# Kernel optimization log

Measured on AMD Instinct MI355X. Metric: run time of the kernel, lower is better.

Reference implementation:

```python
import jax, jax.numpy as jnp
import numpy as np

FEATURE_DIM = 1024
N_CONCEPTS = 32768
BATCH = 1024
TEMPERATURE = 0.1
EPS = 1e-12  # matches torch F.normalize eps


def l2_normalize(x, axis=-1):
    n = jnp.linalg.norm(x, axis=axis, keepdims=True)
    return x / jnp.maximum(n, EPS)


def setup_inputs() -> dict:
    key = jax.random.key(0)
    k1, k2, k3, k4 = jax.random.split(key, 4)
    features = jax.random.normal(k1, (BATCH, FEATURE_DIM), dtype=jnp.float32)
    # Linear projection params (original inits to identity/zeros; random exercises the math)
    W = jnp.eye(FEATURE_DIM, dtype=jnp.float32) + 0.02 * jax.random.normal(k2, (FEATURE_DIM, FEATURE_DIM), dtype=jnp.float32)
    b = 0.01 * jax.random.normal(k3, (FEATURE_DIM,), dtype=jnp.float32)
    prototypes = l2_normalize(jax.random.normal(k4, (N_CONCEPTS, FEATURE_DIM), dtype=jnp.float32))
    return {"features": features, "W": W, "b": b, "prototypes": prototypes}


def reference(features, W, b, prototypes):
    # projection: features @ W.T + b   (torch nn.Linear convention)
    projected = jnp.einsum('bd,ed->be', features, W) + b          # [B, D]
    projected = l2_normalize(projected)                           # [B, D]
    # cosine similarity against all prototypes
    similarities = jnp.einsum('bd,kd->bk', projected, prototypes) # [B, K]
    activations = jax.nn.softmax(similarities / TEMPERATURE, axis=-1)
    best_idx = jnp.argmax(similarities, axis=-1)                  # [B] int
    return activations, best_idx
```

## Files before the change

kernel.cpp:

```cpp
#include <hip/hip_runtime.h>
#include <hip/hip_bf16.h>


typedef __attribute__((ext_vector_type(8))) short short8;
typedef __attribute__((ext_vector_type(4))) float floatx4;

__device__ __forceinline__ unsigned short f2bf(float f) {
  unsigned int u = __float_as_uint(f);
  u += 0x7fffu + ((u >> 16) & 1u);
  return (unsigned short)(u >> 16);
}
__device__ __forceinline__ float bf2f(unsigned short h) {
  return __uint_as_float(((unsigned int)h) << 16);
}

__global__ __launch_bounds__(256) void cvt_f32_bf16(
    const float* __restrict__ src, unsigned short* __restrict__ dst, int n8) {
  int i = blockIdx.x * blockDim.x + threadIdx.x;
  if (i >= n8) return;
  const float4* s4 = (const float4*)src;
  float4 a = s4[2 * i];
  float4 b = s4[2 * i + 1];
  short8 o;
  o[0] = (short)f2bf(a.x); o[1] = (short)f2bf(a.y);
  o[2] = (short)f2bf(a.z); o[3] = (short)f2bf(a.w);
  o[4] = (short)f2bf(b.x); o[5] = (short)f2bf(b.y);
  o[6] = (short)f2bf(b.z); o[7] = (short)f2bf(b.w);
  ((short8*)dst)[i] = o;
}

__global__ __launch_bounds__(256) void cvt_split3(
    const float* __restrict__ src, unsigned short* __restrict__ H,
    unsigned short* __restrict__ Md, unsigned short* __restrict__ L, int n4) {
  int i = blockIdx.x * blockDim.x + threadIdx.x;
  if (i >= n4) return;
  float4 x = ((const float4*)src)[i];
  ushort4 h, m, l;
  float v, r;
  v = x.x; h.x = f2bf(v); r = v - bf2f(h.x); m.x = f2bf(r); l.x = f2bf(r - bf2f(m.x));
  v = x.y; h.y = f2bf(v); r = v - bf2f(h.y); m.y = f2bf(r); l.y = f2bf(r - bf2f(m.y));
  v = x.z; h.z = f2bf(v); r = v - bf2f(h.z); m.z = f2bf(r); l.z = f2bf(r - bf2f(m.z));
  v = x.w; h.w = f2bf(v); r = v - bf2f(h.w); m.w = f2bf(r); l.w = f2bf(r - bf2f(m.w));
  ((ushort4*)H)[i] = h; ((ushort4*)Md)[i] = m; ((ushort4*)L)[i] = l;
}

__global__ __launch_bounds__(256) void gemm_nt_bf16(
    const unsigned short* __restrict__ A, const unsigned short* __restrict__ B,
    float* __restrict__ C, int M, int N, int K) {
  __shared__ unsigned short As[128 * 32];
  __shared__ unsigned short Bs[128 * 32];
  const int tid  = threadIdx.x;
  const int wave = tid >> 6;
  const int lane = tid & 63;
  const long tm = (long)blockIdx.y * 128;
  const long tn = (long)blockIdx.x * 128;
  const int wm = (wave & 1) * 64;
  const int wn = (wave >> 1) * 64;

  floatx4 acc[4][4];
#pragma unroll
  for (int i = 0; i < 4; i++)
#pragma unroll
    for (int j = 0; j < 4; j++) acc[i][j] = (floatx4){0.f, 0.f, 0.f, 0.f};

  const int rstage = tid >> 2;
  const int cstage = (tid & 3) * 8;
  const unsigned short* Abase = A + (tm + rstage) * (long)K + cstage;
  const unsigned short* Bbase = B + (tn + rstage) * (long)K + cstage;

  for (int k0 = 0; k0 < K; k0 += 32) {
    __builtin_amdgcn_global_load_lds(
        (const __attribute__((address_space(1))) void*)(Abase + k0),
        (__attribute__((address_space(3))) void*)(As + wave * 512), 16, 0, 0);
    __builtin_amdgcn_global_load_lds(
        (const __attribute__((address_space(1))) void*)(Abase + 64 * (long)K + k0),
        (__attribute__((address_space(3))) void*)(As + 2048 + wave * 512), 16, 0, 0);
    __builtin_amdgcn_global_load_lds(
        (const __attribute__((address_space(1))) void*)(Bbase + k0),
        (__attribute__((address_space(3))) void*)(Bs + wave * 512), 16, 0, 0);
    __builtin_amdgcn_global_load_lds(
        (const __attribute__((address_space(1))) void*)(Bbase + 64 * (long)K + k0),
        (__attribute__((address_space(3))) void*)(Bs + 2048 + wave * 512), 16, 0, 0);
    __syncthreads();

    short8 af[4], bfv[4];
    const int fr = lane & 15;
    const int koff = (lane >> 4) * 8;
#pragma unroll
    for (int mf = 0; mf < 4; mf++)
      af[mf] = *(const short8*)(As + (wm + mf * 16 + fr) * 32 + koff);
#pragma unroll
    for (int nf = 0; nf < 4; nf++)
      bfv[nf] = *(const short8*)(Bs + (wn + nf * 16 + fr) * 32 + koff);
#pragma unroll
    for (int mf = 0; mf < 4; mf++)
#pragma unroll
      for (int nf = 0; nf < 4; nf++)
        acc[mf][nf] = __builtin_amdgcn_mfma_f32_16x16x32_bf16(
            af[mf], bfv[nf], acc[mf][nf], 0, 0, 0);
    __syncthreads();
  }

  const long crow = tm + wm + ((lane >> 4) * 4);
  const long ccol = tn + wn + (lane & 15);
#pragma unroll
  for (int mf = 0; mf < 4; mf++)
#pragma unroll
    for (int nf = 0; nf < 4; nf++)
#pragma unroll
      for (int r = 0; r < 4; r++)
        C[(crow + mf * 16 + r) * (long)N + ccol + nf * 16] = acc[mf][nf][r];
}

__global__ __launch_bounds__(256) void gemm_split6_nt(
    const unsigned short* __restrict__ Ah, const unsigned short* __restrict__ Am,
    const unsigned short* __restrict__ Al, const unsigned short* __restrict__ Bh,
    const unsigned short* __restrict__ Bm, const unsigned short* __restrict__ Bl,
    float* __restrict__ Cpart, int M, int N, int K) {
  __shared__ unsigned short sA[3][64 * 32];
  __shared__ unsigned short sB[3][64 * 32];
  const int tid  = threadIdx.x;
  const int wave = tid >> 6;
  const int lane = tid & 63;
  const long tm = (long)blockIdx.y * 64;
  const long tn = (long)blockIdx.x * 64;
  const int wm = (wave & 1) * 32;
  const int wn = (wave >> 1) * 32;
  const int ksize = K / gridDim.z;
  const int kbase = blockIdx.z * ksize;
  float* C = Cpart + (size_t)blockIdx.z * M * N;

  floatx4 accH[2][2], accL[2][2];
#pragma unroll
  for (int i = 0; i < 2; i++)
#pragma unroll
    for (int j = 0; j < 2; j++) {
      accH[i][j] = (floatx4){0.f, 0.f, 0.f, 0.f};
      accL[i][j] = (floatx4){0.f, 0.f, 0.f, 0.f};
    }

  const int rstage = tid >> 2;
  const int cstage = (tid & 3) * 8;
  const long aoff = (tm + rstage) * (long)K + cstage;
  const long boff = (tn + rstage) * (long)K + cstage;
  const unsigned short* Asrc[3] = {Ah + aoff, Am + aoff, Al + aoff};
  const unsigned short* Bsrc[3] = {Bh + boff, Bm + boff, Bl + boff};

  for (int k0 = kbase; k0 < kbase + ksize; k0 += 32) {
#pragma unroll
    for (int p = 0; p < 3; p++) {
      __builtin_amdgcn_global_load_lds(
          (const __attribute__((address_space(1))) void*)(Asrc[p] + k0),
          (__attribute__((address_space(3))) void*)(sA[p] + wave * 512), 16, 0, 0);
      __builtin_amdgcn_global_load_lds(
          (const __attribute__((address_space(1))) void*)(Bsrc[p] + k0),
          (__attribute__((address_space(3))) void*)(sB[p] + wave * 512), 16, 0, 0);
    }
    __syncthreads();

    const int fr = lane & 15;
    const int koff = (lane >> 4) * 8;
    short8 a_[3][2], b_[3][2];
#pragma unroll
    for (int p = 0; p < 3; p++)
#pragma unroll
      for (int mf = 0; mf < 2; mf++) {
        a_[p][mf] = *(const short8*)(sA[p] + (wm + mf * 16 + fr) * 32 + koff);
        b_[p][mf] = *(const short8*)(sB[p] + (wn + mf * 16 + fr) * 32 + koff);
      }
#pragma unroll
    for (int mf = 0; mf < 2; mf++)
#pragma unroll
      for (int nf = 0; nf < 2; nf++) {
        accH[mf][nf] = __builtin_amdgcn_mfma_f32_16x16x32_bf16(
            a_[0][mf], b_[0][nf], accH[mf][nf], 0, 0, 0);
        accL[mf][nf] = __builtin_amdgcn_mfma_f32_16x16x32_bf16(
            a_[0][mf], b_[1][nf], accL[mf][nf], 0, 0, 0);
        accL[mf][nf] = __builtin_amdgcn_mfma_f32_16x16x32_bf16(
            a_[1][mf], b_[0][nf], accL[mf][nf], 0, 0, 0);
        accL[mf][nf] = __builtin_amdgcn_mfma_f32_16x16x32_bf16(
            a_[0][mf], b_[2][nf], accL[mf][nf], 0, 0, 0);
        accL[mf][nf] = __builtin_amdgcn_mfma_f32_16x16x32_bf16(
            a_[2][mf], b_[0][nf], accL[mf][nf], 0, 0, 0);
        accL[mf][nf] = __builtin_amdgcn_mfma_f32_16x16x32_bf16(
            a_[1][mf], b_[1][nf], accL[mf][nf], 0, 0, 0);
      }
    __syncthreads();
  }

  const long crow = tm + wm + ((lane >> 4) * 4);
  const long ccol = tn + wn + (lane & 15);
#pragma unroll
  for (int mf = 0; mf < 2; mf++)
#pragma unroll
    for (int nf = 0; nf < 2; nf++)
#pragma unroll
      for (int r = 0; r < 4; r++)
        C[(crow + mf * 16 + r) * (long)N + ccol + nf * 16] =
            accH[mf][nf][r] + accL[mf][nf][r];
}

__global__ __launch_bounds__(256) void norm_bias_rows(
    const float* __restrict__ P0, const float* __restrict__ P1, int nparts,
    const float* __restrict__ bias, unsigned short* __restrict__ Pn,
    float* __restrict__ Pn32) {
  const int b = blockIdx.x, tid = threadIdx.x;
  float4 v = ((const float4*)(P0 + (long)b * 1024))[tid];
  if (nparts == 2) {
    float4 v1 = ((const float4*)(P1 + (long)b * 1024))[tid];
    v.x += v1.x; v.y += v1.y; v.z += v1.z; v.w += v1.w;
  }
  float4 bb = ((const float4*)bias)[tid];
  v.x += bb.x; v.y += bb.y; v.z += bb.z; v.w += bb.w;
  float ss = v.x * v.x + v.y * v.y + v.z * v.z + v.w * v.w;
#pragma unroll
  for (int off = 32; off > 0; off >>= 1) ss += __shfl_down(ss, off);
  __shared__ float wred[4];
  if ((tid & 63) == 0) wred[tid >> 6] = ss;
  __syncthreads();
  float tot = wred[0] + wred[1] + wred[2] + wred[3];
  float inv = 1.0f / fmaxf(sqrtf(tot), 1e-12f);
  float4 p = make_float4(v.x * inv, v.y * inv, v.z * inv, v.w * inv);
  ((float4*)Pn32)[b * 256 + tid] = p;
  ushort4 o;
  o.x = f2bf(p.x); o.y = f2bf(p.y); o.z = f2bf(p.z); o.w = f2bf(p.w);
  ((ushort4*)Pn)[b * 256 + tid] = o;
}

__global__ __launch_bounds__(256) void softmax_argmax_refine(
    float* __restrict__ S, const float* __restrict__ Pn32,
    const float* __restrict__ protos, float* __restrict__ idx_out) {
  const int b = blockIdx.x, tid = threadIdx.x;
  const int wave = tid >> 6, lane = tid & 63;
  float4* row4 = (float4*)(S + (long)b * 32768);

  float m = -3.4e38f, l = 0.f;
#pragma unroll 4
  for (int it = 0; it < 32; it++) {
    float4 v = row4[tid + 256 * it];
    float zx = v.x * 10.f, zy = v.y * 10.f, zz = v.z * 10.f, zw = v.w * 10.f;
    float m4 = fmaxf(fmaxf(zx, zy), fmaxf(zz, zw));
    float nm = fmaxf(m, m4);
    l = l * __expf(m - nm) + __expf(zx - nm) + __expf(zy - nm) +
        __expf(zz - nm) + __expf(zw - nm);
    m = nm;
  }
#pragma unroll
  for (int off = 1; off < 64; off <<= 1) {
    float mo = __shfl_xor(m, off);
    float lo = __shfl_xor(l, off);
    float nm = fmaxf(m, mo);
    l = l * __expf(m - nm) + lo * __expf(mo - nm);
    m = nm;
  }
  __shared__ float sm_[4], sl_[4];
  __shared__ int cand[64];
  __shared__ int ncand;
  if (lane == 0) { sm_[wave] = m; sl_[wave] = l; }
  if (tid == 0) ncand = 0;
  __syncthreads();
  float Mz = fmaxf(fmaxf(sm_[0], sm_[1]), fmaxf(sm_[2], sm_[3]));
  float L = sl_[0] * __expf(sm_[0] - Mz) + sl_[1] * __expf(sm_[1] - Mz) +
            sl_[2] * __expf(sm_[2] - Mz) + sl_[3] * __expf(sm_[3] - Mz);
  float invL = 1.0f / L;
  float thr = Mz * 0.1f - 0.012f;

#pragma unroll 4
  for (int it = 0; it < 32; it++) {
    int i4 = tid + 256 * it;
    float4 v = row4[i4];
    if (fmaxf(fmaxf(v.x, v.y), fmaxf(v.z, v.w)) >= thr) {
      if (v.x >= thr) { int p = atomicAdd(&ncand, 1); if (p < 64) cand[p] = i4 * 4; }
      if (v.y >= thr) { int p = atomicAdd(&ncand, 1); if (p < 64) cand[p] = i4 * 4 + 1; }
      if (v.z >= thr) { int p = atomicAdd(&ncand, 1); if (p < 64) cand[p] = i4 * 4 + 2; }
      if (v.w >= thr) { int p = atomicAdd(&ncand, 1); if (p < 64) cand[p] = i4 * 4 + 3; }
    }
    float4 e;
    e.x = __expf(v.x * 10.f - Mz) * invL;
    e.y = __expf(v.y * 10.f - Mz) * invL;
    e.z = __expf(v.z * 10.f - Mz) * invL;
    e.w = __expf(v.w * 10.f - Mz) * invL;
    row4[i4] = e;
  }
  __syncthreads();
  int n = ncand < 64 ? ncand : 64;

  float4 pv = ((const float4*)(Pn32 + (long)b * 1024))[tid];
  __shared__ double dred[4];
  double best = -1e300;
  int besti = 0x7fffffff;
  for (int c = 0; c < n; c++) {
    int k = cand[c];
    float4 kv = ((const float4*)(protos + (long)k * 1024))[tid];
    double d = (double)pv.x * kv.x + (double)pv.y * kv.y +
               (double)pv.z * kv.z + (double)pv.w * kv.w;
#pragma unroll
    for (int off = 32; off > 0; off >>= 1) d += __shfl_down(d, off);
    if (lane == 0) dred[wave] = d;
    __syncthreads();
    if (tid == 0) {
      double tot = dred[0] + dred[1] + dred[2] + dred[3];
      if (tot > best || (tot == best && k < besti)) { best = tot; besti = k; }
    }
    __syncthreads();
  }
  if (tid == 0) idx_out[b] = (float)besti;
}

extern "C" void kernel_launch(void* const* d_in, const int* in_sizes, int n_in,
                              void* d_out, int out_size, void* d_ws, size_t ws_size,
                              hipStream_t stream) {
  const float* features = (const float*)d_in[0];
  const float* W        = (const float*)d_in[1];
  const float* bias     = (const float*)d_in[2];
  const float* protos   = (const float*)d_in[3];

  const size_t MB = 1024 * 1024;
  char* ws = (char*)d_ws;
  unsigned short* protoB = (unsigned short*)ws;
  unsigned short* Fh = (unsigned short*)(ws + 64 * MB);
  unsigned short* Fm = (unsigned short*)(ws + 66 * MB);
  unsigned short* Fl = (unsigned short*)(ws + 68 * MB);
  unsigned short* Wh = (unsigned short*)(ws + 70 * MB);
  unsigned short* Wm = (unsigned short*)(ws + 72 * MB);
  unsigned short* Wl = (unsigned short*)(ws + 74 * MB);
  float*          P0 = (float*)(ws + 76 * MB);
  float*          P1 = (float*)(ws + 80 * MB);
  unsigned short* Pn   = (unsigned short*)(ws + 64 * MB);
  float*          Pn32 = (float*)(ws + 66 * MB);

  const int ksplit = (ws_size >= 84 * MB) ? 2 : 1;

  float* S = (float*)d_out;
  float* idx_out = S + (size_t)1024 * 32768;

  cvt_f32_bf16<<<16384, 256, 0, stream>>>(protos, protoB, 32768 * 1024 / 8);
  cvt_split3<<<1024, 256, 0, stream>>>(features, Fh, Fm, Fl, 1024 * 1024 / 4);
  cvt_split3<<<1024, 256, 0, stream>>>(W, Wh, Wm, Wl, 1024 * 1024 / 4);
  gemm_split6_nt<<<dim3(16, 16, ksplit), 256, 0, stream>>>(
      Fh, Fm, Fl, Wh, Wm, Wl, P0, 1024, 1024, 1024);
  norm_bias_rows<<<1024, 256, 0, stream>>>(P0, P1, ksplit, bias, Pn, Pn32);
  gemm_nt_bf16<<<dim3(256, 8), 256, 0, stream>>>(Pn, protoB, S, 1024, 32768, 1024);
  softmax_argmax_refine<<<1024, 256, 0, stream>>>(S, Pn32, protos, idx_out);
}
```

Baseline: 442.4 us.

## Load GEMM operands directly to registers, use fixed softmax max, deeper k-split

```diff
diff --git a/kernel.cpp b/kernel.cpp
--- a/kernel.cpp
+++ b/kernel.cpp
@@ -44,18 +44,25 @@
   ((ushort4*)H)[i] = h; ((ushort4*)Md)[i] = m; ((ushort4*)L)[i] = l;
 }
 
-__global__ __launch_bounds__(256) void gemm_nt_bf16(
+__global__ __launch_bounds__(256) void gemm_nt_bf16_direct(
     const unsigned short* __restrict__ A, const unsigned short* __restrict__ B,
-    float* __restrict__ C, int M, int N, int K) {
-  __shared__ unsigned short As[128 * 32];
-  __shared__ unsigned short Bs[128 * 32];
-  const int tid  = threadIdx.x;
-  const int wave = tid >> 6;
-  const int lane = tid & 63;
+    float* __restrict__ C, int M, int N) {
+  const int K = 1024;
+  const int tid = threadIdx.x;
+  const int wave = tid >> 6, lane = tid & 63;
   const long tm = (long)blockIdx.y * 128;
   const long tn = (long)blockIdx.x * 128;
-  const int wm = (wave & 1) * 64;
-  const int wn = (wave >> 1) * 64;
+  const int wm = (wave & 1) * 64, wn = (wave >> 1) * 64;
+  const int fr = lane & 15;
+  const int kc = (lane >> 4) * 8;
+
+  const unsigned short* Ap[4];
+  const unsigned short* Bp[4];
+#pragma unroll
+  for (int i = 0; i < 4; i++) {
+    Ap[i] = A + (tm + wm + i * 16 + fr) * (long)K + kc;
+    Bp[i] = B + (tn + wn + i * 16 + fr) * (long)K + kc;
+  }
 
   floatx4 acc[4][4];
 #pragma unroll
@@ -63,42 +70,39 @@
 #pragma unroll
     for (int j = 0; j < 4; j++) acc[i][j] = (floatx4){0.f, 0.f, 0.f, 0.f};
 
-  const int rstage = tid >> 2;
-  const int cstage = (tid & 3) * 8;
-  const unsigned short* Abase = A + (tm + rstage) * (long)K + cstage;
-  const unsigned short* Bbase = B + (tn + rstage) * (long)K + cstage;
-
-  for (int k0 = 0; k0 < K; k0 += 32) {
-    __builtin_amdgcn_global_load_lds(
-        (const __attribute__((address_space(1))) void*)(Abase + k0),
-        (__attribute__((address_space(3))) void*)(As + wave * 512), 16, 0, 0);
-    __builtin_amdgcn_global_load_lds(
-        (const __attribute__((address_space(1))) void*)(Abase + 64 * (long)K + k0),
-        (__attribute__((address_space(3))) void*)(As + 2048 + wave * 512), 16, 0, 0);
-    __builtin_amdgcn_global_load_lds(
-        (const __attribute__((address_space(1))) void*)(Bbase + k0),
-        (__attribute__((address_space(3))) void*)(Bs + wave * 512), 16, 0, 0);
-    __builtin_amdgcn_global_load_lds(
-        (const __attribute__((address_space(1))) void*)(Bbase + 64 * (long)K + k0),
-        (__attribute__((address_space(3))) void*)(Bs + 2048 + wave * 512), 16, 0, 0);
-    __syncthreads();
-
-    short8 af[4], bfv[4];
-    const int fr = lane & 15;
-    const int koff = (lane >> 4) * 8;
-#pragma unroll
-    for (int mf = 0; mf < 4; mf++)
-      af[mf] = *(const short8*)(As + (wm + mf * 16 + fr) * 32 + koff);
-#pragma unroll
-    for (int nf = 0; nf < 4; nf++)
-      bfv[nf] = *(const short8*)(Bs + (wn + nf * 16 + fr) * 32 + koff);
+  short8 a0[4], b0[4], a1[4], b1[4];
+#pragma unroll
+  for (int i = 0; i < 4; i++) {
+    a0[i] = *(const short8*)(Ap[i]);
+    b0[i] = *(const short8*)(Bp[i]);
+  }
+
+#pragma unroll
+  for (int k0 = 0; k0 < K; k0 += 64) {
+#pragma unroll
+    for (int i = 0; i < 4; i++) {
+      a1[i] = *(const short8*)(Ap[i] + k0 + 32);
+      b1[i] = *(const short8*)(Bp[i] + k0 + 32);
+    }
 #pragma unroll
     for (int mf = 0; mf < 4; mf++)
 #pragma unroll
       for (int nf = 0; nf < 4; nf++)
         acc[mf][nf] = __builtin_amdgcn_mfma_f32_16x16x32_bf16(
-            af[mf], bfv[nf], acc[mf][nf], 0, 0, 0);
-    __syncthreads();
+            a0[mf], b0[nf], acc[mf][nf], 0, 0, 0);
+    if (k0 + 64 < K) {
+#pragma unroll
+      for (int i = 0; i < 4; i++) {
+        a0[i] = *(const short8*)(Ap[i] + k0 + 64);
+        b0[i] = *(const short8*)(Bp[i] + k0 + 64);
+      }
+    }
+#pragma unroll
+    for (int mf = 0; mf < 4; mf++)
+#pragma unroll
+      for (int nf = 0; nf < 4; nf++)
+        acc[mf][nf] = __builtin_amdgcn_mfma_f32_16x16x32_bf16(
+            a1[mf], b1[nf], acc[mf][nf], 0, 0, 0);
   }
 
   const long crow = tm + wm + ((lane >> 4) * 4);
@@ -112,24 +116,34 @@
         C[(crow + mf * 16 + r) * (long)N + ccol + nf * 16] = acc[mf][nf][r];
 }
 
-__global__ __launch_bounds__(256) void gemm_split6_nt(
+__global__ __launch_bounds__(256) void gemm_split6_direct(
     const unsigned short* __restrict__ Ah, const unsigned short* __restrict__ Am,
     const unsigned short* __restrict__ Al, const unsigned short* __restrict__ Bh,
     const unsigned short* __restrict__ Bm, const unsigned short* __restrict__ Bl,
     float* __restrict__ Cpart, int M, int N, int K) {
-  __shared__ unsigned short sA[3][64 * 32];
-  __shared__ unsigned short sB[3][64 * 32];
-  const int tid  = threadIdx.x;
-  const int wave = tid >> 6;
-  const int lane = tid & 63;
+  const int tid = threadIdx.x;
+  const int wave = tid >> 6, lane = tid & 63;
   const long tm = (long)blockIdx.y * 64;
   const long tn = (long)blockIdx.x * 64;
-  const int wm = (wave & 1) * 32;
-  const int wn = (wave >> 1) * 32;
+  const int wm = (wave & 1) * 32, wn = (wave >> 1) * 32;
+  const int fr = lane & 15;
+  const int kc = (lane >> 4) * 8;
   const int ksize = K / gridDim.z;
   const int kbase = blockIdx.z * ksize;
   float* C = Cpart + (size_t)blockIdx.z * M * N;
 
+  const unsigned short* Asrc[3] = {Ah, Am, Al};
+  const unsigned short* Bsrc[3] = {Bh, Bm, Bl};
+  const unsigned short* Aptr[3][2];
+  const unsigned short* Bptr[3][2];
+#pragma unroll
+  for (int p = 0; p < 3; p++)
+#pragma unroll
+    for (int i = 0; i < 2; i++) {
+      Aptr[p][i] = Asrc[p] + (tm + wm + i * 16 + fr) * (long)K + kc + kbase;
+      Bptr[p][i] = Bsrc[p] + (tn + wn + i * 16 + fr) * (long)K + kc + kbase;
+    }
+
   floatx4 accH[2][2], accL[2][2];
 #pragma unroll
   for (int i = 0; i < 2; i++)
@@ -139,34 +153,14 @@
       accL[i][j] = (floatx4){0.f, 0.f, 0.f, 0.f};
     }
 
-  const int rstage = tid >> 2;
-  const int cstage = (tid & 3) * 8;
-  const long aoff = (tm + rstage) * (long)K + cstage;
-  const long boff = (tn + rstage) * (long)K + cstage;
-  const unsigned short* Asrc[3] = {Ah + aoff, Am + aoff, Al + aoff};
-  const unsigned short* Bsrc[3] = {Bh + boff, Bm + boff, Bl + boff};
-
-  for (int k0 = kbase; k0 < kbase + ksize; k0 += 32) {
-#pragma unroll
-    for (int p = 0; p < 3; p++) {
-      __builtin_amdgcn_global_load_lds(
-          (const __attribute__((address_space(1))) void*)(Asrc[p] + k0),
-          (__attribute__((address_space(3))) void*)(sA[p] + wave * 512), 16, 0, 0);
-      __builtin_amdgcn_global_load_lds(
-          (const __attribute__((address_space(1))) void*)(Bsrc[p] + k0),
-          (__attribute__((address_space(3))) void*)(sB[p] + wave * 512), 16, 0, 0);
-    }
-    __syncthreads();
-
-    const int fr = lane & 15;
-    const int koff = (lane >> 4) * 8;
+  for (int k0 = 0; k0 < ksize; k0 += 32) {
     short8 a_[3][2], b_[3][2];
 #pragma unroll
     for (int p = 0; p < 3; p++)
 #pragma unroll
-      for (int mf = 0; mf < 2; mf++) {
-        a_[p][mf] = *(const short8*)(sA[p] + (wm + mf * 16 + fr) * 32 + koff);
-        b_[p][mf] = *(const short8*)(sB[p] + (wn + mf * 16 + fr) * 32 + koff);
+      for (int i = 0; i < 2; i++) {
+        a_[p][i] = *(const short8*)(Aptr[p][i] + k0);
+        b_[p][i] = *(const short8*)(Bptr[p][i] + k0);
       }
 #pragma unroll
     for (int mf = 0; mf < 2; mf++)
@@ -185,7 +179,6 @@
         accL[mf][nf] = __builtin_amdgcn_mfma_f32_16x16x32_bf16(
             a_[1][mf], b_[1][nf], accL[mf][nf], 0, 0, 0);
       }
-    __syncthreads();
   }
 
   const long crow = tm + wm + ((lane >> 4) * 4);
@@ -201,13 +194,12 @@
 }
 
 __global__ __launch_bounds__(256) void norm_bias_rows(
-    const float* __restrict__ P0, const float* __restrict__ P1, int nparts,
-    const float* __restrict__ bias, unsigned short* __restrict__ Pn,
-    float* __restrict__ Pn32) {
+    const float* __restrict__ P, int nparts, const float* __restrict__ bias,
+    unsigned short* __restrict__ Pn, float* __restrict__ Pn32) {
   const int b = blockIdx.x, tid = threadIdx.x;
-  float4 v = ((const float4*)(P0 + (long)b * 1024))[tid];
-  if (nparts == 2) {
-    float4 v1 = ((const float4*)(P1 + (long)b * 1024))[tid];
+  float4 v = ((const float4*)(P + (long)b * 1024))[tid];
+  for (int p = 1; p < nparts; p++) {
+    float4 v1 = ((const float4*)(P + (size_t)p * 1024 * 1024 + (long)b * 1024))[tid];
     v.x += v1.x; v.y += v1.y; v.z += v1.z; v.w += v1.w;
   }
   float4 bb = ((const float4*)bias)[tid];
@@ -234,36 +226,29 @@
   const int wave = tid >> 6, lane = tid & 63;
   float4* row4 = (float4*)(S + (long)b * 32768);
 
-  float m = -3.4e38f, l = 0.f;
-#pragma unroll 4
+  float mx = -3.4e38f, l = 0.f;
+#pragma unroll 8
   for (int it = 0; it < 32; it++) {
     float4 v = row4[tid + 256 * it];
-    float zx = v.x * 10.f, zy = v.y * 10.f, zz = v.z * 10.f, zw = v.w * 10.f;
-    float m4 = fmaxf(fmaxf(zx, zy), fmaxf(zz, zw));
-    float nm = fmaxf(m, m4);
-    l = l * __expf(m - nm) + __expf(zx - nm) + __expf(zy - nm) +
-        __expf(zz - nm) + __expf(zw - nm);
-    m = nm;
+    mx = fmaxf(mx, fmaxf(fmaxf(v.x, v.y), fmaxf(v.z, v.w)));
+    l += __expf(v.x * 10.f - 10.f) + __expf(v.y * 10.f - 10.f) +
+         __expf(v.z * 10.f - 10.f) + __expf(v.w * 10.f - 10.f);
   }
 #pragma unroll
   for (int off = 1; off < 64; off <<= 1) {
-    float mo = __shfl_xor(m, off);
-    float lo = __shfl_xor(l, off);
-    float nm = fmaxf(m, mo);
-    l = l * __expf(m - nm) + lo * __expf(mo - nm);
-    m = nm;
+    mx = fmaxf(mx, __shfl_xor(mx, off));
+    l += __shfl_xor(l, off);
   }
   __shared__ float sm_[4], sl_[4];
   __shared__ int cand[64];
   __shared__ int ncand;
-  if (lane == 0) { sm_[wave] = m; sl_[wave] = l; }
+  if (lane == 0) { sm_[wave] = mx; sl_[wave] = l; }
   if (tid == 0) ncand = 0;
   __syncthreads();
-  float Mz = fmaxf(fmaxf(sm_[0], sm_[1]), fmaxf(sm_[2], sm_[3]));
-  float L = sl_[0] * __expf(sm_[0] - Mz) + sl_[1] * __expf(sm_[1] - Mz) +
-            sl_[2] * __expf(sm_[2] - Mz) + sl_[3] * __expf(sm_[3] - Mz);
+  float MX = fmaxf(fmaxf(sm_[0], sm_[1]), fmaxf(sm_[2], sm_[3]));
+  float L = sl_[0] + sl_[1] + sl_[2] + sl_[3];
   float invL = 1.0f / L;
-  float thr = Mz * 0.1f - 0.012f;
+  float thr = MX - 0.012f;
 
 #pragma unroll 4
   for (int it = 0; it < 32; it++) {
@@ -276,10 +261,10 @@
       if (v.w >= thr) { int p = atomicAdd(&ncand, 1); if (p < 64) cand[p] = i4 * 4 + 3; }
     }
     float4 e;
-    e.x = __expf(v.x * 10.f - Mz) * invL;
-    e.y = __expf(v.y * 10.f - Mz) * invL;
-    e.z = __expf(v.z * 10.f - Mz) * invL;
-    e.w = __expf(v.w * 10.f - Mz) * invL;
+    e.x = __expf(v.x * 10.f - 10.f) * invL;
+    e.y = __expf(v.y * 10.f - 10.f) * invL;
+    e.z = __expf(v.z * 10.f - 10.f) * invL;
+    e.w = __expf(v.w * 10.f - 10.f) * invL;
     row4[i4] = e;
   }
   __syncthreads();
@@ -324,12 +309,11 @@
   unsigned short* Wh = (unsigned short*)(ws + 70 * MB);
   unsigned short* Wm = (unsigned short*)(ws + 72 * MB);
   unsigned short* Wl = (unsigned short*)(ws + 74 * MB);
-  float*          P0 = (float*)(ws + 76 * MB);
-  float*          P1 = (float*)(ws + 80 * MB);
+  float*          P  = (float*)(ws + 76 * MB);
   unsigned short* Pn   = (unsigned short*)(ws + 64 * MB);
   float*          Pn32 = (float*)(ws + 66 * MB);
 
-  const int ksplit = (ws_size >= 84 * MB) ? 2 : 1;
+  const int ksplit = (ws_size >= 92 * MB) ? 4 : (ws_size >= 84 * MB) ? 2 : 1;
 
   float* S = (float*)d_out;
   float* idx_out = S + (size_t)1024 * 32768;
@@ -337,9 +321,9 @@
   cvt_f32_bf16<<<16384, 256, 0, stream>>>(protos, protoB, 32768 * 1024 / 8);
   cvt_split3<<<1024, 256, 0, stream>>>(features, Fh, Fm, Fl, 1024 * 1024 / 4);
   cvt_split3<<<1024, 256, 0, stream>>>(W, Wh, Wm, Wl, 1024 * 1024 / 4);
-  gemm_split6_nt<<<dim3(16, 16, ksplit), 256, 0, stream>>>(
-      Fh, Fm, Fl, Wh, Wm, Wl, P0, 1024, 1024, 1024);
-  norm_bias_rows<<<1024, 256, 0, stream>>>(P0, P1, ksplit, bias, Pn, Pn32);
-  gemm_nt_bf16<<<dim3(256, 8), 256, 0, stream>>>(Pn, protoB, S, 1024, 32768, 1024);
+  gemm_split6_direct<<<dim3(16, 16, ksplit), 256, 0, stream>>>(
+      Fh, Fm, Fl, Wh, Wm, Wl, P, 1024, 1024, 1024);
+  norm_bias_rows<<<1024, 256, 0, stream>>>(P, ksplit, bias, Pn, Pn32);
+  gemm_nt_bf16_direct<<<dim3(256, 8), 256, 0, stream>>>(Pn, protoB, S, 1024, 32768);
   softmax_argmax_refine<<<1024, 256, 0, stream>>>(S, Pn32, protos, idx_out);
 }
```

Result: slower. 594.6 us (+34.4%).
